# Optimization experiments

Hardware: AMD Instinct MI355X
Metric: run time of the kernel (lower is better)

## Reference

```python
import jax, jax.numpy as jnp
import numpy as np

B, L, D = 4, 1024, 1024
DI, DS, DC, DR = 2048, 16, 4, 64  # d_inner, d_state, d_conv, dt_rank


def setup_inputs() -> dict:
    key = jax.random.key(0)
    ks = jax.random.split(key, 24)
    rn = lambda k, shape, s=0.02: s * jax.random.normal(k, shape, jnp.float32)
    inp = {"x": jax.random.normal(ks[0], (B, L, D), jnp.float32)}
    for i, p in enumerate(("f", "b")):
        o = 1 + i * 8
        inp[f"in_proj_{p}"] = rn(ks[o], (2 * DI, D))
        inp[f"conv_w_{p}"] = rn(ks[o + 1], (DI, DC), 0.2)
        inp[f"conv_b_{p}"] = rn(ks[o + 2], (DI,), 0.1)
        inp[f"x_proj_{p}"] = rn(ks[o + 3], (DR + 2 * DS, DI))
        inp[f"dt_w_{p}"] = rn(ks[o + 4], (DI, DR), 0.1)
        inp[f"dt_b_{p}"] = rn(ks[o + 5], (DI,), 0.5)
        inp[f"A_log_{p}"] = jnp.log(jnp.broadcast_to(jnp.arange(1.0, DS + 1.0, dtype=jnp.float32), (DI, DS))) + 0.0
        inp[f"D_{p}"] = jnp.ones((DI,), jnp.float32)
        inp[f"out_proj_{p}"] = rn(ks[o + 6], (D, DI))
    inp["ln_w"] = jnp.ones((D,), jnp.float32)
    inp["ln_b"] = jnp.zeros((D,), jnp.float32)
    return inp


def _mamba(x, in_proj, conv_w, conv_b, x_proj, dt_w, dt_b, A_log, Dsk, out_proj):
    # x: [B, L, D]
    xz = x @ in_proj.T                      # [B, L, 2*DI]
    xh, z = jnp.split(xz, 2, axis=-1)        # each [B, L, DI]
    # causal depthwise conv1d (left-pad DC-1), fused silu
    xp = jnp.pad(xh, ((0, 0), (DC - 1, 0), (0, 0)))
    Ls = xh.shape[1]
    xc = conv_b + sum(xp[:, k:k + Ls, :] * conv_w[:, k] for k in range(DC))
    xc = jax.nn.silu(xc)
    # input-dependent dt, B, C
    dbc = xc @ x_proj.T                      # [B, L, DR+2*DS]
    dt, Bm, Cm = jnp.split(dbc, [DR, DR + DS], axis=-1)
    delta = jax.nn.softplus(dt @ dt_w.T + dt_b)  # [B, L, DI]
    A = -jnp.exp(A_log)                      # [DI, DS]

    def step(h, inp):
        u_t, d_t, B_t, C_t = inp             # [B,DI],[B,DI],[B,DS],[B,DS]
        h = h * jnp.exp(d_t[:, :, None] * A) + (d_t * u_t)[:, :, None] * B_t[:, None, :]
        return h, jnp.einsum('bds,bs->bd', h, C_t)

    inps = (jnp.moveaxis(xc, 1, 0), jnp.moveaxis(delta, 1, 0),
            jnp.moveaxis(Bm, 1, 0), jnp.moveaxis(Cm, 1, 0))
    h0 = jnp.zeros((x.shape[0], DI, DS), x.dtype)
    _, ys = jax.lax.scan(step, h0, inps)     # ys: [L, B, DI]
    y = jnp.moveaxis(ys, 0, 1) + xc * Dsk
    y = y * jax.nn.silu(z)
    return y @ out_proj.T                    # [B, L, D]


def reference(x,
              in_proj_f, conv_w_f, conv_b_f, x_proj_f, dt_w_f, dt_b_f, A_log_f, D_f, out_proj_f,
              in_proj_b, conv_w_b, conv_b_b, x_proj_b, dt_w_b, dt_b_b, A_log_b, D_b, out_proj_b,
              ln_w, ln_b):
    yf = _mamba(x, in_proj_f, conv_w_f, conv_b_f, x_proj_f, dt_w_f, dt_b_f, A_log_f, D_f, out_proj_f)
    yb = jnp.flip(_mamba(jnp.flip(x, 1), in_proj_b, conv_w_b, conv_b_b, x_proj_b, dt_w_b, dt_b_b, A_log_b, D_b, out_proj_b), 1)
    h = x + yf + yb
    mu = jnp.mean(h, axis=-1, keepdims=True)
    var = jnp.mean(jnp.square(h - mu), axis=-1, keepdims=True)
    return (h - mu) / jnp.sqrt(var + 1e-5) * ln_w + ln_b
```

## Files before the change

kernel.cpp:

```cpp
#include <hip/hip_runtime.h>
#include <cstdint>
#include <cstddef>

#define BB  4
#define LL  1024
#define DD  1024
#define DIN 2048
#define DS  16
#define DC  4
#define DR  64

typedef unsigned short ushort_t;
typedef __attribute__((ext_vector_type(8))) short bf16x8;
typedef __attribute__((ext_vector_type(4))) float f32x4;
typedef __attribute__((ext_vector_type(4))) unsigned short us4;

enum { EPI_STORE = 0, EPI_ADD = 1, EPI_BIAS_SOFTPLUS = 2 };

__device__ __forceinline__ float softplus_f(float v) {
  return (v > 20.f) ? v : log1pf(expf(v));
}
__device__ __forceinline__ float silu_f(float v) {
  return v / (1.f + expf(-v));
}
__device__ __forceinline__ ushort_t f32_to_bf16(float f) {
  uint32_t u = __float_as_uint(f);
  uint32_t r = (u + 0x7FFFu + ((u >> 16) & 1u)) >> 16;
  return (ushort_t)r;
}
__device__ __forceinline__ float bf16_to_f32(ushort_t u) {
  return __uint_as_float(((uint32_t)u) << 16);
}

__device__ __forceinline__ void async_copy16(const void* g, void* lds) {
  __builtin_amdgcn_global_load_lds(
      (const __attribute__((address_space(1))) unsigned int*)g,
      (__attribute__((address_space(3))) unsigned int*)lds, 16, 0, 0);
}

__global__ __launch_bounds__(256) void cast_bf16_kernel(
    const float* __restrict__ src, ushort_t* __restrict__ dst, int n)
{
  int i = (blockIdx.x * 256 + threadIdx.x) * 4;
  if (i >= n) return;
  float4 v = *(const float4*)(src + i);
  us4 o = { f32_to_bf16(v.x), f32_to_bf16(v.y), f32_to_bf16(v.z), f32_to_bf16(v.w) };
  *(us4*)(dst + i) = o;
}

__global__ __launch_bounds__(256) void cast_pad_bf16_kernel(
    const float* __restrict__ src, ushort_t* __restrict__ dst,
    int srcRows, int dstRows, int cols)
{
  int i = (blockIdx.x * 256 + threadIdx.x) * 4;
  if (i >= dstRows * cols) return;
  int row = i / cols;
  us4 o = {0, 0, 0, 0};
  if (row < srcRows) {
    float4 v = *(const float4*)(src + (size_t)row * cols + (i % cols));
    o = (us4){ f32_to_bf16(v.x), f32_to_bf16(v.y), f32_to_bf16(v.z), f32_to_bf16(v.w) };
  }
  *(us4*)(dst + i) = o;
}

template<int EPI, int OBF>
__global__ __launch_bounds__(256) void gemm_nt_mfma(
    const ushort_t* __restrict__ A, int lda,
    const ushort_t* __restrict__ B, int ldb,
    void* C, int ldc, const float* __restrict__ bias, int K)
{
  __shared__ __align__(16) ushort_t As[128 * 32];
  __shared__ __align__(16) ushort_t Bs[128 * 32];
  const int tid  = threadIdx.x;
  const int lane = tid & 63;
  const int wave = tid >> 6;
  const int wm = (wave & 1) * 64;
  const int wn = (wave >> 1) * 64;
  const int m0 = blockIdx.x * 128;
  const int n0 = blockIdx.y * 128;
  const int lr = lane & 15;
  const int lk = (lane >> 4) * 8;

  f32x4 acc[4][4];
#pragma unroll
  for (int i = 0; i < 4; ++i)
#pragma unroll
    for (int j = 0; j < 4; ++j) acc[i][j] = (f32x4){0.f, 0.f, 0.f, 0.f};

  for (int k0 = 0; k0 < K; k0 += 32) {
    __syncthreads();
#pragma unroll
    for (int it = 0; it < 2; ++it) {
      int c  = tid + it * 256;
      int r  = c >> 2;
      int cb = (c & 3) << 3;
      async_copy16(A + (size_t)(m0 + r) * lda + k0 + cb, (char*)As + c * 16);
      async_copy16(B + (size_t)(n0 + r) * ldb + k0 + cb, (char*)Bs + c * 16);
    }
    __syncthreads();

    bf16x8 a_frag[4], b_frag[4];
#pragma unroll
    for (int i = 0; i < 4; ++i)
      a_frag[i] = *(const bf16x8*)&As[(wm + i * 16 + lr) * 32 + lk];
#pragma unroll
    for (int j = 0; j < 4; ++j)
      b_frag[j] = *(const bf16x8*)&Bs[(wn + j * 16 + lr) * 32 + lk];
#pragma unroll
    for (int i = 0; i < 4; ++i)
#pragma unroll
      for (int j = 0; j < 4; ++j)
        acc[i][j] = __builtin_amdgcn_mfma_f32_16x16x32_bf16(
            a_frag[i], b_frag[j], acc[i][j], 0, 0, 0);
  }

  const int rbase = m0 + wm + (lane >> 4) * 4;
  const int cbase = n0 + wn + (lane & 15);
#pragma unroll
  for (int i = 0; i < 4; ++i)
#pragma unroll
    for (int j = 0; j < 4; ++j)
#pragma unroll
      for (int r = 0; r < 4; ++r) {
        size_t off = (size_t)(rbase + i * 16 + r) * ldc + cbase + j * 16;
        float v = acc[i][j][r];
        if (EPI == EPI_ADD) v += ((float*)C)[off];
        if (EPI == EPI_BIAS_SOFTPLUS) v = softplus_f(v + bias[cbase + j * 16]);
        if (OBF) ((ushort_t*)C)[off] = f32_to_bf16(v);
        else     ((float*)C)[off] = v;
      }
}

__global__ __launch_bounds__(256) void conv_silu_kernel(
    const ushort_t* __restrict__ xz,
    const float* __restrict__ w,
    const float* __restrict__ bias,
    ushort_t* __restrict__ xc,
    int reverse)
{
  int idx = blockIdx.x * 256 + threadIdx.x;
  if (idx >= BB * LL * DIN) return;
  int d = idx & (DIN - 1);
  int t = (idx >> 11) & (LL - 1);
  int b = idx >> 21;
  const float4 wv = *(const float4*)(w + d * 4);
  const float wj[4] = {wv.x, wv.y, wv.z, wv.w};
  float acc = bias[d];
#pragma unroll
  for (int j = 0; j < 4; ++j) {
    int pos = reverse ? (t + 3 - j) : (t - 3 + j);
    if (pos >= 0 && pos < LL)
      acc = fmaf(bf16_to_f32(xz[(size_t)(b * LL + pos) * 4096 + d]), wj[j], acc);
  }
  xc[idx] = f32_to_bf16(silu_f(acc));
}

#define SCAN_U 16
__global__ __launch_bounds__(256) void scan_kernel(
    const float* __restrict__ delta,
    const ushort_t* __restrict__ xcb,
    const ushort_t* __restrict__ dbc,
    const ushort_t* __restrict__ xzb,
    const float* __restrict__ A_log,
    const float* __restrict__ Dsk,
    ushort_t* __restrict__ ybf,
    int reverse)
{
  const int tid = threadIdx.x;
  const int s = tid & 15;
  const int ch = blockIdx.x * 16 + (tid >> 4);
  const int b = ch >> 11;
  const int d = ch & (DIN - 1);
  const float As2 = -expf(A_log[d * DS + s]) * 1.44269504088896f;
  const float Dv = Dsk[d];
  const int t0 = reverse ? (LL - 1) : 0;
  const int dt = reverse ? -1 : 1;
  const size_t rowbase = (size_t)b * LL;

  float h = 0.f;
  for (int i0 = 0; i0 < LL; i0 += SCAN_U) {
    float dl[SCAN_U], uu[SCAN_U], Bv[SCAN_U], Cv[SCAN_U], zz[SCAN_U];
#pragma unroll
    for (int k = 0; k < SCAN_U; ++k) {
      const size_t row = rowbase + (size_t)(t0 + dt * (i0 + k));
      dl[k] = delta[row * DIN + d];
      uu[k] = bf16_to_f32(xcb[row * DIN + d]);
      Bv[k] = bf16_to_f32(dbc[row * 128 + DR + s]);
      Cv[k] = bf16_to_f32(dbc[row * 128 + DR + DS + s]);
      zz[k] = bf16_to_f32(xzb[row * 4096 + DIN + d]);
    }
#pragma unroll
    for (int k = 0; k < SCAN_U; ++k) {
      float a = exp2f(dl[k] * As2);
      h = fmaf(h, a, (dl[k] * uu[k]) * Bv[k]);
      float p = h * Cv[k];
      p += __shfl_xor(p, 1, 16);
      p += __shfl_xor(p, 2, 16);
      p += __shfl_xor(p, 4, 16);
      p += __shfl_xor(p, 8, 16);
      if (s == 0) {
        const size_t row = rowbase + (size_t)(t0 + dt * (i0 + k));
        ybf[row * DIN + d] = f32_to_bf16((p + uu[k] * Dv) * silu_f(zz[k]));
      }
    }
  }
}

__global__ __launch_bounds__(256) void ln_kernel(
    const float* __restrict__ x, const float* __restrict__ accum,
    const float* __restrict__ lnw, const float* __restrict__ lnb,
    float* __restrict__ out)
{
  int row = blockIdx.x;
  int tid = threadIdx.x;
  size_t base = (size_t)row * DD + tid * 4;
  float4 xv = *(const float4*)(x + base);
  float4 av = *(const float4*)(accum + base);
  float h0 = xv.x + av.x, h1 = xv.y + av.y;
  float h2 = xv.z + av.z, h3 = xv.w + av.w;
  float s = h0 + h1 + h2 + h3;
  float q = h0 * h0 + h1 * h1 + h2 * h2 + h3 * h3;
#pragma unroll
  for (int m = 1; m < 64; m <<= 1) {
    s += __shfl_xor(s, m, 64);
    q += __shfl_xor(q, m, 64);
  }
  __shared__ float rs[4], rq[4];
  int wid = tid >> 6;
  if ((tid & 63) == 0) { rs[wid] = s; rq[wid] = q; }
  __syncthreads();
  s = rs[0] + rs[1] + rs[2] + rs[3];
  q = rq[0] + rq[1] + rq[2] + rq[3];
  float mu = s * (1.f / DD);
  float var = q * (1.f / DD) - mu * mu;
  float rstd = rsqrtf(var + 1e-5f);
  float4 w  = *(const float4*)(lnw + tid * 4);
  float4 bv = *(const float4*)(lnb + tid * 4);
  float4 o;
  o.x = (h0 - mu) * rstd * w.x + bv.x;
  o.y = (h1 - mu) * rstd * w.y + bv.y;
  o.z = (h2 - mu) * rstd * w.z + bv.z;
  o.w = (h3 - mu) * rstd * w.w + bv.w;
  *(float4*)(out + base) = o;
}

extern "C" void kernel_launch(void* const* d_in, const int* in_sizes, int n_in,
                              void* d_out, int out_size, void* d_ws, size_t ws_size,
                              hipStream_t stream) {
  const float* x = (const float*)d_in[0];
  const float* P[2][9];
  for (int dir = 0; dir < 2; ++dir)
    for (int j = 0; j < 9; ++j)
      P[dir][j] = (const float*)d_in[1 + dir * 9 + j];
  const float* ln_w = (const float*)d_in[19];
  const float* ln_b = (const float*)d_in[20];
  float* out = (float*)d_out;
  (void)ws_size;

  const size_t F = 1024 * 1024;
  float* ws = (float*)d_ws;
  ushort_t* XZBF  = (ushort_t*)(ws);
  ushort_t* XCBF  = (ushort_t*)(ws + 8  * F);
  ushort_t* DBC   = (ushort_t*)(ws + 12 * F);
  float*    DELTA = ws + 13 * F;
  float*    ACC   = ws + 21 * F;
  ushort_t* XBF   = (ushort_t*)(ws + 25 * F);
  ushort_t* WBF   = (ushort_t*)(ws + 27 * F);
  ushort_t* OPBF  = (ushort_t*)(ws + 31 * F);
  ushort_t* XPBF  = (ushort_t*)(ws + 33 * F);
  ushort_t* DTWBF = (ushort_t*)(ws + 33 * F + F / 2);
  ushort_t* YBF   = (ushort_t*)(ws + 34 * F);

  const int MROWS = BB * LL;

  cast_bf16_kernel<<<(MROWS * DD) / 1024, 256, 0, stream>>>(x, XBF, MROWS * DD);

  for (int dir = 0; dir < 2; ++dir) {
    const float* in_proj  = P[dir][0];
    const float* conv_w   = P[dir][1];
    const float* conv_b   = P[dir][2];
    const float* x_proj   = P[dir][3];
    const float* dt_w     = P[dir][4];
    const float* dt_b     = P[dir][5];
    const float* A_log    = P[dir][6];
    const float* Dsk      = P[dir][7];
    const float* out_proj = P[dir][8];

    cast_bf16_kernel<<<(2 * DIN * DD) / 1024, 256, 0, stream>>>(
        in_proj, WBF, 2 * DIN * DD);
    cast_pad_bf16_kernel<<<(128 * DIN) / 1024, 256, 0, stream>>>(
        x_proj, XPBF, DR + 2 * DS, 128, DIN);
    cast_bf16_kernel<<<(DIN * DR) / 1024, 256, 0, stream>>>(
        dt_w, DTWBF, DIN * DR);

    gemm_nt_mfma<EPI_STORE, 1><<<dim3(32, 32), 256, 0, stream>>>(
        XBF, DD, WBF, DD, XZBF, 2 * DIN, nullptr, DD);

    conv_silu_kernel<<<(BB * LL * DIN) / 256, 256, 0, stream>>>(
        XZBF, conv_w, conv_b, XCBF, dir);

    gemm_nt_mfma<EPI_STORE, 1><<<dim3(32, 1), 256, 0, stream>>>(
        XCBF, DIN, XPBF, DIN, DBC, 128, nullptr, DIN);

    gemm_nt_mfma<EPI_BIAS_SOFTPLUS, 0><<<dim3(32, 16), 256, 0, stream>>>(
        DBC, 128, DTWBF, DR, DELTA, DIN, dt_b, DR);

    scan_kernel<<<512, 256, 0, stream>>>(
        DELTA, XCBF, DBC, XZBF, A_log, Dsk, YBF, dir);

    cast_bf16_kernel<<<(DD * DIN) / 1024, 256, 0, stream>>>(
        out_proj, OPBF, DD * DIN);
    if (dir == 0)
      gemm_nt_mfma<EPI_STORE, 0><<<dim3(32, 8), 256, 0, stream>>>(
          YBF, DIN, OPBF, DIN, ACC, DD, nullptr, DIN);
    else
      gemm_nt_mfma<EPI_ADD, 0><<<dim3(32, 8), 256, 0, stream>>>(
          YBF, DIN, OPBF, DIN, ACC, DD, nullptr, DIN);
  }

  ln_kernel<<<MROWS, 256, 0, stream>>>(x, ACC, ln_w, ln_b, out);
}
```

Baseline: 1.237 ms.

## Split selective scan into chunked two-pass parallel scan

Replaces the single sequential scan over all 1024 timesteps with a two-pass chunked scan. The sequence is cut into 8 chunks. A partial kernel computes each chunk's decay product and local state, and a final kernel combines the earlier chunk summaries as a prefix and then rescans its own chunk to emit outputs. This aims to fix the latency-bound scan that launched only 512 blocks, by giving 8x more parallel blocks. The cost is reading delta, xc and B twice, plus an extra launch and small summary buffers.

After: 1.106 ms. 10.5% less time.

```diff
diff --git a/kernel.cpp b/kernel.cpp
--- a/kernel.cpp
+++ b/kernel.cpp
@@ -9,6 +9,9 @@
 #define DS  16
 #define DC  4
 #define DR  64
+
+#define NCHUNK 8
+#define CS (LL / NCHUNK)
 
 typedef unsigned short ushort_t;
 typedef __attribute__((ext_vector_type(8))) short bf16x8;
@@ -155,20 +158,64 @@
   xc[idx] = f32_to_bf16(silu_f(acc));
 }
 
-#define SCAN_U 16
-__global__ __launch_bounds__(256) void scan_kernel(
+__global__ __launch_bounds__(256) void scan_partial_kernel(
+    const float* __restrict__ delta,
+    const ushort_t* __restrict__ xcb,
+    const ushort_t* __restrict__ dbc,
+    const float* __restrict__ A_log,
+    float* __restrict__ Asum,
+    float* __restrict__ Hsum,
+    int reverse)
+{
+  const int tid = threadIdx.x;
+  const int s = tid & 15;
+  const int ch = blockIdx.x * 16 + (tid >> 4);
+  const int cc = blockIdx.y;
+  const int b = ch >> 11;
+  const int d = ch & (DIN - 1);
+  const float As2 = -expf(A_log[d * DS + s]) * 1.44269504088896f;
+  const int t0 = reverse ? (LL - 1) : 0;
+  const int dt = reverse ? -1 : 1;
+  const size_t rowbase = (size_t)b * LL;
+
+  float h = 0.f, Ap = 1.f;
+  for (int i0 = cc * CS; i0 < (cc + 1) * CS; i0 += 8) {
+    float dl[8], uu[8], Bv[8];
+#pragma unroll
+    for (int k = 0; k < 8; ++k) {
+      const size_t row = rowbase + (size_t)(t0 + dt * (i0 + k));
+      dl[k] = delta[row * DIN + d];
+      uu[k] = bf16_to_f32(xcb[row * DIN + d]);
+      Bv[k] = bf16_to_f32(dbc[row * 128 + DR + s]);
+    }
+#pragma unroll
+    for (int k = 0; k < 8; ++k) {
+      float a = exp2f(dl[k] * As2);
+      h = fmaf(h, a, (dl[k] * uu[k]) * Bv[k]);
+      Ap *= a;
+    }
+  }
+  const size_t off = ((size_t)ch * NCHUNK + cc) * 16 + s;
+  Asum[off] = Ap;
+  Hsum[off] = h;
+}
+
+__global__ __launch_bounds__(256) void scan_final_kernel(
     const float* __restrict__ delta,
     const ushort_t* __restrict__ xcb,
     const ushort_t* __restrict__ dbc,
     const ushort_t* __restrict__ xzb,
     const float* __restrict__ A_log,
     const float* __restrict__ Dsk,
+    const float* __restrict__ Asum,
+    const float* __restrict__ Hsum,
     ushort_t* __restrict__ ybf,
     int reverse)
 {
   const int tid = threadIdx.x;
   const int s = tid & 15;
   const int ch = blockIdx.x * 16 + (tid >> 4);
+  const int cc = blockIdx.y;
   const int b = ch >> 11;
   const int d = ch & (DIN - 1);
   const float As2 = -expf(A_log[d * DS + s]) * 1.44269504088896f;
@@ -178,10 +225,15 @@
   const size_t rowbase = (size_t)b * LL;
 
   float h = 0.f;
-  for (int i0 = 0; i0 < LL; i0 += SCAN_U) {
-    float dl[SCAN_U], uu[SCAN_U], Bv[SCAN_U], Cv[SCAN_U], zz[SCAN_U];
-#pragma unroll
-    for (int k = 0; k < SCAN_U; ++k) {
+  for (int c = 0; c < cc; ++c) {
+    const size_t off = ((size_t)ch * NCHUNK + c) * 16 + s;
+    h = fmaf(Asum[off], h, Hsum[off]);
+  }
+
+  for (int i0 = cc * CS; i0 < (cc + 1) * CS; i0 += 8) {
+    float dl[8], uu[8], Bv[8], Cv[8], zz[8];
+#pragma unroll
+    for (int k = 0; k < 8; ++k) {
       const size_t row = rowbase + (size_t)(t0 + dt * (i0 + k));
       dl[k] = delta[row * DIN + d];
       uu[k] = bf16_to_f32(xcb[row * DIN + d]);
@@ -190,7 +242,7 @@
       zz[k] = bf16_to_f32(xzb[row * 4096 + DIN + d]);
     }
 #pragma unroll
-    for (int k = 0; k < SCAN_U; ++k) {
+    for (int k = 0; k < 8; ++k) {
       float a = exp2f(dl[k] * As2);
       h = fmaf(h, a, (dl[k] * uu[k]) * Bv[k]);
       float p = h * Cv[k];
@@ -270,6 +322,8 @@
   ushort_t* XPBF  = (ushort_t*)(ws + 33 * F);
   ushort_t* DTWBF = (ushort_t*)(ws + 33 * F + F / 2);
   ushort_t* YBF   = (ushort_t*)(ws + 34 * F);
+  float*    ASUM  = ws + 38 * F;
+  float*    HSUM  = ws + 39 * F;
 
   const int MROWS = BB * LL;
 
@@ -305,8 +359,10 @@
     gemm_nt_mfma<EPI_BIAS_SOFTPLUS, 0><<<dim3(32, 16), 256, 0, stream>>>(
         DBC, 128, DTWBF, DR, DELTA, DIN, dt_b, DR);
 
-    scan_kernel<<<512, 256, 0, stream>>>(
-        DELTA, XCBF, DBC, XZBF, A_log, Dsk, YBF, dir);
+    scan_partial_kernel<<<dim3(512, NCHUNK), 256, 0, stream>>>(
+        DELTA, XCBF, DBC, A_log, ASUM, HSUM, dir);
+    scan_final_kernel<<<dim3(512, NCHUNK), 256, 0, stream>>>(
+        DELTA, XCBF, DBC, XZBF, A_log, Dsk, ASUM, HSUM, YBF, dir);
 
     cast_bf16_kernel<<<(DD * DIN) / 1024, 256, 0, stream>>>(
         out_proj, OPBF, DD * DIN);
```
